# Kernel optimization log

Hardware: AMD Instinct MI355X
Metric: run time of the kernel (lower is better)

Reference implementation:

```python
import jax, jax.numpy as jnp
import numpy as np

NUM_HEADS = 16
EPS = 1e-12  # matches torch F.normalize eps


def _l2norm(t):
    n = jnp.sqrt(jnp.sum(t * t, axis=-1, keepdims=True))
    return t / jnp.maximum(n, EPS)


def setup_inputs() -> dict:
    key = jax.random.key(0)
    kx, kq, kk, kv = jax.random.split(key, 4)
    B, S, E = 2, 2048, 1024
    head_dim = E // NUM_HEADS
    bound = 1.0 / np.sqrt(E)  # nn.Linear default init range
    x = jax.random.normal(kx, (B, S, E), dtype=jnp.float32)
    Wq = jax.random.uniform(kq, (E, E), dtype=jnp.float32, minval=-bound, maxval=bound)
    Wk = jax.random.uniform(kk, (E, E), dtype=jnp.float32, minval=-bound, maxval=bound)
    Wv = jax.random.uniform(kv, (E, E), dtype=jnp.float32, minval=-bound, maxval=bound)
    g_scale = jnp.asarray(np.sqrt(head_dim), dtype=jnp.float32)  # 1/d_k = sqrt(head_dim)
    return {"x": x, "Wq": Wq, "Wk": Wk, "Wv": Wv, "g_scale": g_scale}


def reference(x, Wq, Wk, Wv, g_scale):
    B, S, E = x.shape
    H = NUM_HEADS
    D = E // H
    # projections (torch Linear: x @ W.T), split heads -> [B, H, S, D]
    q = (x @ Wq.T).reshape(B, S, H, D).transpose(0, 2, 1, 3)
    k = (x @ Wk.T).reshape(B, S, H, D).transpose(0, 2, 1, 3)
    v = (x @ Wv.T).reshape(B, S, H, D).transpose(0, 2, 1, 3)
    # qk_norm branch: L2-normalize q, k then learnable scale
    q = _l2norm(q)
    k = _l2norm(k)
    scores = g_scale * jnp.einsum('bhqd,bhkd->bhqk', q, k)  # [B, H, S, S]
    attn = jax.nn.softmax(scores, axis=-1)
    # dropout p=0.0 (eval) -> identity
    out = jnp.einsum('bhqk,bhkd->bhqd', attn, v)  # [B, H, S, D]
    out = out.transpose(0, 2, 1, 3).reshape(B, S, E)
    return out
```

## Files before the change

kernel.cpp:

```cpp
#include <hip/hip_runtime.h>
#include <math.h>

#define NH 16
#define HD 64
#define SEQ 2048
#define BAT 2
#define EMB 1024
#define MTOT (BAT*SEQ)
#define NTOT (3*EMB)

typedef __attribute__((ext_vector_type(8))) short bf16x8;
typedef __attribute__((ext_vector_type(4))) float f32x4;

#define MFMA16(a,b,c) __builtin_amdgcn_mfma_f32_16x16x32_bf16(a,b,c,0,0,0)

__device__ inline short f2bf(float f) {
    union { float f; unsigned u; } x; x.f = f;
    unsigned r = (x.u + 0x7FFF + ((x.u >> 16) & 1)) >> 16;
    return (short)r;
}

__device__ inline float fast_exp2(float x) {
#if __has_builtin(__builtin_amdgcn_exp2f)
    return __builtin_amdgcn_exp2f(x);
#else
    float r; asm("v_exp_f32 %0, %1" : "=v"(r) : "v"(x)); return r;
#endif
}

__device__ inline unsigned pack2bf(float a, float b) {
    union { float f; unsigned u; } x, y; x.f = a; y.f = b;
    return __builtin_amdgcn_perm(y.u + 0x8000u, x.u + 0x8000u, 0x07060302u);
}

typedef const __attribute__((address_space(1))) void* gp_t;
typedef __attribute__((address_space(3))) void* lp_t;
__device__ inline void gload16(const void* g, void* l) {
    __builtin_amdgcn_global_load_lds((gp_t)(uintptr_t)g, (lp_t)(uintptr_t)l, 16, 0, 0);
}

__global__ __launch_bounds__(256) void prep_kernel(
    const float* __restrict__ x, const float* __restrict__ wq,
    const float* __restrict__ wk, const float* __restrict__ wv,
    short* __restrict__ xb, short* __restrict__ wb)
{
    const size_t NX = (size_t)MTOT * EMB;
    const size_t NW = (size_t)EMB * EMB;
    const size_t i4 = ((size_t)blockIdx.x * 256 + threadIdx.x) * 4;
    float4 v; short* dst;
    if (i4 < NX) { v = *(const float4*)(x + i4); dst = xb + i4; }
    else {
        size_t j = i4 - NX;
        const float* s = (j < NW) ? wq : (j < 2 * NW) ? wk : wv;
        v = *(const float4*)(s + (j & (NW - 1)));
        dst = wb + j;
    }
    short4 o; o.x = f2bf(v.x); o.y = f2bf(v.y); o.z = f2bf(v.z); o.w = f2bf(v.w);
    *(short4*)dst = o;
}

__global__ __launch_bounds__(256) void qkv_gemm_fast(
    const short* __restrict__ xb, const short* __restrict__ wb,
    short* __restrict__ qws, short* __restrict__ kws, short* __restrict__ vperm,
    const float* __restrict__ gptr)
{
    __shared__ short As[128 * 64];
    __shared__ short Bs[128 * 64];
    const int id = blockIdx.x;
    const int xcd = id & 7, q8 = id >> 3;
    const int m0 = (xcd * 4 + (q8 & 3)) * 128;
    const int n0 = (q8 >> 2) * 128;
    const int t = threadIdx.x, wave = t >> 6, lane = t & 63;
    const int quad = lane >> 4, l16 = lane & 15;
    const int wm = (wave & 1) * 64, wn = (wave >> 1) * 64;

    const int srow = wave * 32 + (lane >> 3);
    const int scol = ((lane & 7) ^ (srow & 7)) * 8;
    const short* ga = xb + (size_t)(m0 + srow) * EMB + scol;
    const short* gb = wb + (size_t)(n0 + srow) * EMB + scol;
    short* lA = As + (size_t)wave * 2048;
    short* lB = Bs + (size_t)wave * 2048;

    const short* Aa[2]; const short* Ba[2];
#pragma unroll
    for (int ks = 0; ks < 2; ++ks) {
        const int pc = (ks * 32 + quad * 8) ^ ((l16 & 7) * 8);
        Aa[ks] = As + (wm + l16) * 64 + pc;
        Ba[ks] = Bs + (wn + l16) * 64 + pc;
    }

    f32x4 acc[4][4] = {};

    for (int k0 = 0; k0 < EMB; k0 += 64) {
#pragma unroll
        for (int j = 0; j < 4; ++j) {
            gload16(ga + k0 + (size_t)j * 8 * EMB, lA + j * 512);
            gload16(gb + k0 + (size_t)j * 8 * EMB, lB + j * 512);
        }
        __syncthreads();
#pragma unroll
        for (int ks = 0; ks < 2; ++ks) {
            bf16x8 af[4], bfr[4];
#pragma unroll
            for (int i = 0; i < 4; ++i) af[i]  = *(const bf16x8*)(Aa[ks] + i * 1024);
#pragma unroll
            for (int i = 0; i < 4; ++i) bfr[i] = *(const bf16x8*)(Ba[ks] + i * 1024);
#pragma unroll
            for (int mf = 0; mf < 4; ++mf)
#pragma unroll
                for (int nf = 0; nf < 4; ++nf)
                    acc[mf][nf] = MFMA16(af[mf], bfr[nf], acc[mf][nf]);
        }
        __syncthreads();
    }

    const int mat = n0 >> 10;
    if (mat < 2) {
        const float scale = (mat == 0) ? gptr[0] * 1.4426950408889634f : 1.0f;
        float inv[4][4];
#pragma unroll
        for (int mf = 0; mf < 4; ++mf)
#pragma unroll
            for (int reg = 0; reg < 4; ++reg) {
                float ss = 0.f;
#pragma unroll
                for (int nf = 0; nf < 4; ++nf) { float v = acc[mf][nf][reg]; ss += v * v; }
                ss += __shfl_xor(ss, 1, 16);
                ss += __shfl_xor(ss, 2, 16);
                ss += __shfl_xor(ss, 4, 16);
                ss += __shfl_xor(ss, 8, 16);
                inv[mf][reg] = scale / fmaxf(sqrtf(ss), 1e-12f);
            }
        short* outp = (mat == 0) ? qws : kws;
#pragma unroll
        for (int mf = 0; mf < 4; ++mf)
#pragma unroll
            for (int nf = 0; nf < 4; ++nf) {
                const int cw = (n0 & 1023) + wn + nf * 16 + l16;
                const int h = cw >> 6, d = cw & 63;
#pragma unroll
                for (int reg = 0; reg < 4; ++reg) {
                    const int s = m0 + wm + mf * 16 + quad * 4 + reg;
                    const int b = s >> 11, sl = s & (SEQ - 1);
                    outp[(((size_t)(b * NH + h) * SEQ + sl) * HD) + d] =
                        f2bf(acc[mf][nf][reg] * inv[mf][reg]);
                }
            }
    } else {
#pragma unroll
        for (int mf = 0; mf < 4; ++mf)
#pragma unroll
            for (int nf = 0; nf < 4; ++nf) {
                const int cw = (n0 & 1023) + wn + nf * 16 + l16;
                const int h = cw >> 6, d = cw & 63;
                const int s = m0 + wm + mf * 16 + quad * 4;
                const int b = s >> 11, sl = s & (SEQ - 1);
                const int pos = (sl & ~31) + ((sl & 12) >> 2) * 8 + ((sl >> 4) & 1) * 4;
                short4 o;
                o.x = f2bf(acc[mf][nf][0]); o.y = f2bf(acc[mf][nf][1]);
                o.z = f2bf(acc[mf][nf][2]); o.w = f2bf(acc[mf][nf][3]);
                *(short4*)&vperm[(((size_t)(b * NH + h) * HD + d) * SEQ) + pos] = o;
            }
    }
}

__global__ __launch_bounds__(256) void attn_kernel(
    const short* __restrict__ qws, const short* __restrict__ kws,
    const short* __restrict__ vperm, float* __restrict__ out)
{
    __shared__ short Kt[2][64 * 64];
    __shared__ short Vt[2][64 * 64];
    const int id = blockIdx.x;
    const int bh = id & 31, qt = id >> 5;
    const int b = bh >> 4, h = bh & (NH - 1);
    const size_t base = (size_t)bh * SEQ * HD;
    const int t = threadIdx.x, wave = t >> 6, lane = t & 63;
    const int quad = lane >> 4, l16 = lane & 15;

    bf16x8 bq[2][2];
    {
        const short* qp = qws + base + (size_t)(qt * 128 + wave * 32 + l16) * HD + quad * 8;
        bq[0][0] = *(const bf16x8*)(qp);
        bq[0][1] = *(const bf16x8*)(qp + 32);
        bq[1][0] = *(const bf16x8*)(qp + 16 * HD);
        bq[1][1] = *(const bf16x8*)(qp + 16 * HD + 32);
    }
    bf16x8 ones;
#pragma unroll
    for (int i = 0; i < 8; ++i) ones[i] = (short)0x3F80;

    const int krow = wave * 16 + (lane >> 3);
    const int kcol = ((lane & 7) ^ (krow & 7)) * 8;
    const int vl8 = lane & 7;

    int pcK[2], pcV[2];
#pragma unroll
    for (int ks = 0; ks < 2; ++ks)
        pcK[ks] = l16 * 64 + ((ks * 32 + quad * 8) ^ ((l16 & 7) * 8));
#pragma unroll
    for (int g = 0; g < 2; ++g)
        pcV[g] = l16 * 64 + (((g * 4 + quad) ^ (l16 & 7)) * 8);

    f32x4 o_acc[2][4] = {};
    f32x4 l_acc[2] = {};

    auto stage = [&](int kt, int p) {
        const short* kg = kws + base + (size_t)(kt * 64 + krow) * HD + kcol;
        short* lK = &Kt[p][0] + (size_t)wave * 1024;
        short* lV = &Vt[p][0] + (size_t)wave * 1024;
#pragma unroll
        for (int j = 0; j < 2; ++j)
            gload16(kg + (size_t)j * 8 * HD, lK + j * 512);
#pragma unroll
        for (int j = 0; j < 2; ++j) {
            const int d = krow + j * 8;
            const int lg = vl8 ^ (d & 7);
            gload16(vperm + base + (size_t)d * SEQ + kt * 64 + lg * 8, lV + j * 512);
        }
    };

    stage(0, 0);
    __syncthreads();

    for (int kt = 0; kt < SEQ / 64; ++kt) {
        const int p = kt & 1;
        if (kt + 1 < SEQ / 64) stage(kt + 1, p ^ 1);
        const short* Kp = &Kt[p][0];
        const short* Vp = &Vt[p][0];

#pragma unroll
        for (int g = 0; g < 2; ++g) {
            f32x4 st[2][2];
#pragma unroll
            for (int pp = 0; pp < 2; ++pp) {
                const int tau = 2 * g + pp;
                bf16x8 a0 = *(const bf16x8*)(Kp + pcK[0] + tau * 1024);
                bf16x8 a1 = *(const bf16x8*)(Kp + pcK[1] + tau * 1024);
#pragma unroll
                for (int qs = 0; qs < 2; ++qs) {
                    f32x4 z = {};
                    z = MFMA16(a0, bq[qs][0], z);
                    st[pp][qs] = MFMA16(a1, bq[qs][1], z);
                }
            }
            bf16x8 vf[4];
#pragma unroll
            for (int nt = 0; nt < 4; ++nt)
                vf[nt] = *(const bf16x8*)(Vp + pcV[g] + nt * 1024);
#pragma unroll
            for (int qs = 0; qs < 2; ++qs) {
                bf16x8 pa;
                unsigned* pu = (unsigned*)&pa;
                pu[0] = pack2bf(fast_exp2(st[0][qs][0]), fast_exp2(st[0][qs][1]));
                pu[1] = pack2bf(fast_exp2(st[0][qs][2]), fast_exp2(st[0][qs][3]));
                pu[2] = pack2bf(fast_exp2(st[1][qs][0]), fast_exp2(st[1][qs][1]));
                pu[3] = pack2bf(fast_exp2(st[1][qs][2]), fast_exp2(st[1][qs][3]));
                l_acc[qs] = MFMA16(pa, ones, l_acc[qs]);
#pragma unroll
                for (int nt = 0; nt < 4; ++nt)
                    o_acc[qs][nt] = MFMA16(pa, vf[nt], o_acc[qs][nt]);
            }
        }
        __syncthreads();
    }

    float linv[2][4];
#pragma unroll
    for (int qs = 0; qs < 2; ++qs)
#pragma unroll
        for (int r = 0; r < 4; ++r)
            linv[qs][r] = 1.0f / l_acc[qs][r];

    float* ob = out + ((size_t)b * SEQ + qt * 128 + wave * 32 + quad * 4) * EMB + h * HD + l16;
#pragma unroll
    for (int qs = 0; qs < 2; ++qs)
#pragma unroll
        for (int nt = 0; nt < 4; ++nt)
#pragma unroll
            for (int r = 0; r < 4; ++r)
                ob[(size_t)(qs * 16 + r) * EMB + nt * 16] = o_acc[qs][nt][r] * linv[qs][r];
}

extern "C" void kernel_launch(void* const* d_in, const int* in_sizes, int n_in,
                              void* d_out, int out_size, void* d_ws, size_t ws_size,
                              hipStream_t stream) {
    (void)in_sizes; (void)n_in; (void)out_size; (void)ws_size;
    const float* x  = (const float*)d_in[0];
    const float* Wq = (const float*)d_in[1];
    const float* Wk = (const float*)d_in[2];
    const float* Wv = (const float*)d_in[3];
    const float* g  = (const float*)d_in[4];
    float* out = (float*)d_out;

    const size_t per = (size_t)BAT * NH * SEQ * HD;
    short* qws   = (short*)d_ws;
    short* kws   = qws + per;
    short* vperm = kws + per;

    short* xb = (short*)out;
    short* wb = xb + (size_t)MTOT * EMB;

    prep_kernel<<<7168, 256, 0, stream>>>(x, Wq, Wk, Wv, xb, wb);
    qkv_gemm_fast<<<(MTOT / 128) * (NTOT / 128), 256, 0, stream>>>(
        xb, wb, qws, kws, vperm, g);
    attn_kernel<<<(SEQ / 128) * BAT * NH, 256, 0, stream>>>(qws, kws, vperm, out);
}
```

Baseline: 164.1 us.

## Halve attention query tile to 64 rows per block and double grid size

Each attention block now covers 64 query rows (16 per wave) instead of 128, so the grid grows from 512 to 1024 blocks and per-thread register use for accumulators and scores drops by half. Launch bounds now request 4 blocks per CU to encourage higher occupancy. The intent is better CU fill and latency hiding on a GPU with many CUs. In exchange, each K/V tile loaded into shared memory is reused by half as many queries, which doubles total K/V global and LDS traffic.

```diff
diff --git a/kernel.cpp b/kernel.cpp
--- a/kernel.cpp
+++ b/kernel.cpp
@@ -164,7 +164,7 @@
     }
 }
 
-__global__ __launch_bounds__(256) void attn_kernel(
+__global__ __launch_bounds__(256, 4) void attn_kernel(
     const short* __restrict__ qws, const short* __restrict__ kws,
     const short* __restrict__ vperm, float* __restrict__ out)
 {
@@ -177,13 +177,11 @@
     const int t = threadIdx.x, wave = t >> 6, lane = t & 63;
     const int quad = lane >> 4, l16 = lane & 15;
 
-    bf16x8 bq[2][2];
+    bf16x8 bq[2];
     {
-        const short* qp = qws + base + (size_t)(qt * 128 + wave * 32 + l16) * HD + quad * 8;
-        bq[0][0] = *(const bf16x8*)(qp);
-        bq[0][1] = *(const bf16x8*)(qp + 32);
-        bq[1][0] = *(const bf16x8*)(qp + 16 * HD);
-        bq[1][1] = *(const bf16x8*)(qp + 16 * HD + 32);
+        const short* qp = qws + base + (size_t)(qt * 64 + wave * 16 + l16) * HD + quad * 8;
+        bq[0] = *(const bf16x8*)(qp);
+        bq[1] = *(const bf16x8*)(qp + 32);
     }
     bf16x8 ones;
 #pragma unroll
@@ -201,8 +199,8 @@
     for (int g = 0; g < 2; ++g)
         pcV[g] = l16 * 64 + (((g * 4 + quad) ^ (l16 & 7)) * 8);
 
-    f32x4 o_acc[2][4] = {};
-    f32x4 l_acc[2] = {};
+    f32x4 o_acc[4] = {};
+    f32x4 l_acc = {};
 
     auto stage = [&](int kt, int p) {
         const short* kg = kws + base + (size_t)(kt * 64 + krow) * HD + kcol;
@@ -230,55 +228,46 @@
 
 #pragma unroll
         for (int g = 0; g < 2; ++g) {
-            f32x4 st[2][2];
+            f32x4 st[2];
 #pragma unroll
             for (int pp = 0; pp < 2; ++pp) {
                 const int tau = 2 * g + pp;
                 bf16x8 a0 = *(const bf16x8*)(Kp + pcK[0] + tau * 1024);
                 bf16x8 a1 = *(const bf16x8*)(Kp + pcK[1] + tau * 1024);
-#pragma unroll
-                for (int qs = 0; qs < 2; ++qs) {
-                    f32x4 z = {};
-                    z = MFMA16(a0, bq[qs][0], z);
-                    st[pp][qs] = MFMA16(a1, bq[qs][1], z);
-                }
+                f32x4 z = {};
+                z = MFMA16(a0, bq[0], z);
+                st[pp] = MFMA16(a1, bq[1], z);
             }
             bf16x8 vf[4];
 #pragma unroll
             for (int nt = 0; nt < 4; ++nt)
                 vf[nt] = *(const bf16x8*)(Vp + pcV[g] + nt * 1024);
-#pragma unroll
-            for (int qs = 0; qs < 2; ++qs) {
-                bf16x8 pa;
-                unsigned* pu = (unsigned*)&pa;
-                pu[0] = pack2bf(fast_exp2(st[0][qs][0]), fast_exp2(st[0][qs][1]));
-                pu[1] = pack2bf(fast_exp2(st[0][qs][2]), fast_exp2(st[0][qs][3]));
-                pu[2] = pack2bf(fast_exp2(st[1][qs][0]), fast_exp2(st[1][qs][1]));
-                pu[3] = pack2bf(fast_exp2(st[1][qs][2]), fast_exp2(st[1][qs][3]));
-                l_acc[qs] = MFMA16(pa, ones, l_acc[qs]);
-#pragma unroll
-                for (int nt = 0; nt < 4; ++nt)
-                    o_acc[qs][nt] = MFMA16(pa, vf[nt], o_acc[qs][nt]);
-            }
+
+            bf16x8 pa;
+            unsigned* pu = (unsigned*)&pa;
+            pu[0] = pack2bf(fast_exp2(st[0][0]), fast_exp2(st[0][1]));
+            pu[1] = pack2bf(fast_exp2(st[0][2]), fast_exp2(st[0][3]));
+            pu[2] = pack2bf(fast_exp2(st[1][0]), fast_exp2(st[1][1]));
+            pu[3] = pack2bf(fast_exp2(st[1][2]), fast_exp2(st[1][3]));
+            l_acc = MFMA16(pa, ones, l_acc);
+#pragma unroll
+            for (int nt = 0; nt < 4; ++nt)
+                o_acc[nt] = MFMA16(pa, vf[nt], o_acc[nt]);
         }
         __syncthreads();
     }
 
-    float linv[2][4];
-#pragma unroll
-    for (int qs = 0; qs < 2; ++qs)
+    float linv[4];
+#pragma unroll
+    for (int r = 0; r < 4; ++r)
+        linv[r] = 1.0f / l_acc[r];
+
+    float* ob = out + ((size_t)b * SEQ + qt * 64 + wave * 16 + quad * 4) * EMB + h * HD + l16;
+#pragma unroll
+    for (int nt = 0; nt < 4; ++nt)
 #pragma unroll
         for (int r = 0; r < 4; ++r)
-            linv[qs][r] = 1.0f / l_acc[qs][r];
-
-    float* ob = out + ((size_t)b * SEQ + qt * 128 + wave * 32 + quad * 4) * EMB + h * HD + l16;
-#pragma unroll
-    for (int qs = 0; qs < 2; ++qs)
-#pragma unroll
-        for (int nt = 0; nt < 4; ++nt)
-#pragma unroll
-            for (int r = 0; r < 4; ++r)
-                ob[(size_t)(qs * 16 + r) * EMB + nt * 16] = o_acc[qs][nt][r] * linv[qs][r];
+            ob[(size_t)r * EMB + nt * 16] = o_acc[nt][r] * linv[r];
 }
 
 extern "C" void kernel_launch(void* const* d_in, const int* in_sizes, int n_in,
@@ -303,5 +292,5 @@
     prep_kernel<<<7168, 256, 0, stream>>>(x, Wq, Wk, Wv, xb, wb);
     qkv_gemm_fast<<<(MTOT / 128) * (NTOT / 128), 256, 0, stream>>>(
         xb, wb, qws, kws, vperm, g);
-    attn_kernel<<<(SEQ / 128) * BAT * NH, 256, 0, stream>>>(qws, kws, vperm, out);
-}
+    attn_kernel<<<(SEQ / 64) * BAT * NH, 256, 0, stream>>>(qws, kws, vperm, out);
+}
```

Measured after the change: 163.9 us. About the same (-0.1%).
